# Optimization experiments

Measured on AMD Instinct MI355X. Metric: run time of the kernel, lower is better.

## Reference

```python
import jax, jax.numpy as jnp
import numpy as np

B, S, D = 4, 4096, 64

def setup_inputs() -> dict:
    key = jax.random.key(0)
    ks = jax.random.split(key, 6)
    mk = lambda k: jax.random.normal(k, (B, S, D), dtype=jnp.float32)
    return {
        "q_re": mk(ks[0]), "q_im": mk(ks[1]),
        "k_re": mk(ks[2]), "k_im": mk(ks[3]),
        "v_re": mk(ks[4]), "v_im": mk(ks[5]),
    }

def reference(q_re, q_im, k_re, k_im, v_re, v_im):
    # Complex QK^T (no conjugate, matching torch.bmm on complex tensors):
    # (qr + i qi)(kr + i ki)^T -> re = qr kr^T - qi ki^T ; im = qr ki^T + qi kr^T
    d_k = q_re.shape[-1]
    scale = 1.0 / jnp.sqrt(jnp.asarray(d_k, dtype=q_re.dtype))
    s_re = (jnp.einsum('bqd,bkd->bqk', q_re, k_re)
            - jnp.einsum('bqd,bkd->bqk', q_im, k_im)) * scale
    s_im = (jnp.einsum('bqd,bkd->bqk', q_re, k_im)
            + jnp.einsum('bqd,bkd->bqk', q_im, k_re)) * scale
    # softmax over |scores| along key axis; weights are real (imag part is 0)
    w = jax.nn.softmax(jnp.sqrt(s_re * s_re + s_im * s_im), axis=-1)  # [B,S,S]
    # CVDropout is identity in eval mode. Output = real_weights @ complex_values
    o_re = jnp.einsum('bqk,bkd->bqd', w, v_re)
    o_im = jnp.einsum('bqk,bkd->bqd', w, v_im)
    return jnp.stack([o_re, o_im], axis=0)  # [2, B, S, D] (real, imag)
```

## Files before the change

### kernel.cpp

```cpp
#include <hip/hip_runtime.h>
#include <stdint.h>

#define B_    4
#define S_    4096
#define D_    64
#define QBLK  64
#define KVBLK 64
#define NT    (S_ / KVBLK)
#define NELEM (B_ * S_ * D_)
#define BS_   (B_ * S_)

typedef __attribute__((ext_vector_type(8))) short bf16x8;
typedef __attribute__((ext_vector_type(4))) short bf16x4;
typedef __attribute__((ext_vector_type(4))) float f32x4;
typedef __attribute__((ext_vector_type(4))) int   i32x4;
typedef __attribute__((ext_vector_type(4))) unsigned u32x4;
typedef __attribute__((ext_vector_type(4))) _Float16 f16x4;

#define MFMA(a, b, c) __builtin_amdgcn_mfma_f32_16x16x32_bf16(a, b, c, 0, 0, 0)
#define VMWAIT(n) asm volatile("s_waitcnt vmcnt(" #n ")" ::: "memory")
#define BARRIER() do { asm volatile("" ::: "memory"); __builtin_amdgcn_s_barrier(); asm volatile("" ::: "memory"); } while (0)
#define LGKM_FENCE() do { asm volatile("s_waitcnt lgkmcnt(0)" ::: "memory"); __builtin_amdgcn_sched_barrier(0); } while (0)

__device__ __forceinline__ short f2bf(float x) {
    unsigned u = __builtin_bit_cast(unsigned, x);
    u += 0x7FFFu + ((u >> 16) & 1u);
    return (short)(u >> 16);
}

__device__ __forceinline__ unsigned cvtpk(float lo, float hi) {
    unsigned r;
    asm("v_cvt_pk_bf16_f32 %0, %1, %2" : "=v"(r) : "v"(lo), "v"(hi));
    return r;
}

__device__ __forceinline__ void async16(const short* g, short* l) {
    __builtin_amdgcn_global_load_lds(
        (const __attribute__((address_space(1))) unsigned int*)g,
        (__attribute__((address_space(3))) unsigned int*)l, 16, 0, 0);
}

__global__ __launch_bounds__(256)
void prepass_kernel(const float* __restrict__ q_re, const float* __restrict__ q_im,
                    const float* __restrict__ k_re, const float* __restrict__ k_im,
                    const float* __restrict__ v_re, const float* __restrict__ v_im,
                    short* __restrict__ ws) {
    const int bidx = blockIdx.x;
    const int tid  = threadIdx.x;
    if (bidx < 4096) {
        const int idx = bidx * 256 + tid;
        const int tn  = idx >> 18;
        const int e4  = idx & ((1 << 18) - 1);
        const float* s = (tn == 0 ? q_re : tn == 1 ? q_im : tn == 2 ? k_re : k_im)
                         + (size_t)e4 * 4;
        const float sc = (tn < 2) ? 0.125f : 1.0f;
        f32x4 x = *(const f32x4*)s;
        bf16x4 v;
#pragma unroll
        for (int c = 0; c < 4; ++c) v[c] = f2bf(x[c] * sc);
        *(bf16x4*)(ws + (size_t)tn * NELEM + (size_t)e4 * 4) = v;
    } else {
        __shared__ short tile[64][72];
        const int tb   = bidx - 4096;
        const int sb   = tb & 63;
        const int b    = (tb >> 6) & 3;
        const int comp = tb >> 8;
        const float* src = comp ? v_im : v_re;
        short* dst = ws + (size_t)(4 + comp) * NELEM;
#pragma unroll
        for (int i = 0; i < 4; ++i) {
            const int slot = i * 256 + tid;
            const int s  = slot >> 4;
            const int d4 = slot & 15;
            f32x4 x = *(const f32x4*)(src + (((size_t)b * S_) + sb * 64 + s) * D_ + d4 * 4);
#pragma unroll
            for (int c = 0; c < 4; ++c) tile[d4 * 4 + c][s] = f2bf(x[c]);
        }
        __syncthreads();
#pragma unroll
        for (int i = 0; i < 2; ++i) {
            const int slot = i * 256 + tid;
            const int d = slot >> 3;
            const int m = slot & 7;
            const int a = m >> 2, hh = m & 3;
            bf16x8 v;
#pragma unroll
            for (int j = 0; j < 8; ++j)
                v[j] = tile[d][a * 32 + hh * 4 + ((j >> 2) << 4) + (j & 3)];
            *(bf16x8*)(dst + ((size_t)b * 64 + d) * S_ + sb * 64 + m * 8) = v;
        }
    }
}

template<int SPLIT, typename OT>
__global__ __launch_bounds__(256, 2)
void cv_attn_main(const short* __restrict__ wsb,
                  float* __restrict__ out,
                  OT* __restrict__ opart,
                  float* __restrict__ ml)
{
    __shared__ __align__(16) short smem[2 * 4 * KVBLK * D_];

    const int tid  = threadIdx.x;
    const int lane = tid & 63;
    const int wv   = tid >> 6;
    const int l15  = lane & 15;
    const int h    = lane >> 4;

    int bid = blockIdx.x;
    const int nwg = B_ * 64 * SPLIT;
    bid = (bid & 7) * (nwg >> 3) + (bid >> 3);
    const int qb = bid & 63;
    const int sp = (bid >> 6) % SPLIT;
    const int b  = bid / (64 * SPLIT);

    const short* qr  = wsb;
    const short* qi  = wsb + (size_t)NELEM;
    const short* kr  = wsb + 2 * (size_t)NELEM;
    const short* ki  = wsb + 3 * (size_t)NELEM;
    const short* vrT = wsb + 4 * (size_t)NELEM;
    const short* viT = wsb + 5 * (size_t)NELEM;

    short* kb0 = smem + l15 * 64 + ((h ^ (l15 & 7)) << 3);
    short* kb1 = smem + l15 * 64 + (((h ^ 4) ^ (l15 & 7)) << 3);

    const int qrow = qb * QBLK + wv * 16 + l15;
    const size_t qoff = ((size_t)b * S_ + qrow) * D_;
    bf16x8 fqr[2], fqi[2], fqn[2];
#pragma unroll
    for (int dh = 0; dh < 2; ++dh) {
        fqr[dh] = *(const bf16x8*)(qr + qoff + dh * 32 + h * 8);
        fqi[dh] = *(const bf16x8*)(qi + qoff + dh * 32 + h * 8);
        i32x4 n = __builtin_bit_cast(i32x4, fqi[dh]) ^ (int)0x80008000;
        fqn[dh] = __builtin_bit_cast(bf16x8, n);
    }

    f32x4 o_re[4], o_im[4];
#pragma unroll
    for (int i = 0; i < 4; ++i) {
        o_re[i] = (f32x4){0.f, 0.f, 0.f, 0.f};
        o_im[i] = (f32x4){0.f, 0.f, 0.f, 0.f};
    }
    float m_run = -1e30f, l_run = 0.f;
    const float L2E = 1.44269504088896f;

    const int r8   = lane >> 3;
    const int u16l = lane & 7;
    constexpr int TPB = NT / SPLIT;

    auto stage = [&](int t, int DST) {
        const int kb = (sp * TPB + t) * KVBLK;
#pragma unroll
        for (int i = 0; i < 2; ++i) {
            const int row   = wv * 16 + i * 8 + r8;
            const int lbase = (wv * 16 + i * 8) * 64;
            const int swz   = (u16l ^ (row & 7)) << 3;
            const size_t koff = ((size_t)b * S_ + kb + row) * 64 + swz;
            async16(kr + koff, smem + DST + lbase);
            async16(ki + koff, smem + DST + 4096 + lbase);
            const size_t voff = ((size_t)b * 64 + row) * S_ + kb + swz;
            async16(vrT + voff, smem + DST + 8192 + lbase);
            async16(viT + voff, smem + DST + 12288 + lbase);
        }
    };

    auto body = [&](int t, int CUR, int OTH) {
        VMWAIT(0);
        LGKM_FENCE();
        BARRIER();
        if (t + 1 < TPB) stage(t + 1, OTH);

        f32x4 s_re[4], s_im[4];
#pragma unroll
        for (int c = 0; c < 4; ++c) {
            s_re[c] = (f32x4){0.f, 0.f, 0.f, 0.f};
            s_im[c] = (f32x4){0.f, 0.f, 0.f, 0.f};
        }
        __builtin_amdgcn_s_setprio(1);
#pragma unroll
        for (int c = 0; c < 4; ++c) {
            bf16x8 fkr0 = *(const bf16x8*)(kb0 + CUR + c * 1024);
            bf16x8 fkr1 = *(const bf16x8*)(kb1 + CUR + c * 1024);
            bf16x8 fki0 = *(const bf16x8*)(kb0 + CUR + 4096 + c * 1024);
            bf16x8 fki1 = *(const bf16x8*)(kb1 + CUR + 4096 + c * 1024);
            s_re[c] = MFMA(fkr0, fqr[0], s_re[c]);
            s_re[c] = MFMA(fkr1, fqr[1], s_re[c]);
            s_re[c] = MFMA(fki0, fqn[0], s_re[c]);
            s_re[c] = MFMA(fki1, fqn[1], s_re[c]);
            s_im[c] = MFMA(fki0, fqr[0], s_im[c]);
            s_im[c] = MFMA(fki1, fqr[1], s_im[c]);
            s_im[c] = MFMA(fkr0, fqi[0], s_im[c]);
            s_im[c] = MFMA(fkr1, fqi[1], s_im[c]);
        }
        __builtin_amdgcn_s_setprio(0);

#pragma unroll
        for (int c = 0; c < 4; ++c) {
            f32x4 g = s_re[c] * s_re[c] + s_im[c] * s_im[c];
#pragma unroll
            for (int r = 0; r < 4; ++r) s_re[c][r] = __builtin_amdgcn_sqrtf(g[r]);
        }
        float tmax = s_re[0][0];
#pragma unroll
        for (int c = 0; c < 4; ++c)
#pragma unroll
            for (int r = 0; r < 4; ++r) tmax = fmaxf(tmax, s_re[c][r]);
        tmax = fmaxf(tmax, __shfl_xor(tmax, 16));
        tmax = fmaxf(tmax, __shfl_xor(tmax, 32));

        if (__any(tmax > m_run + 8.0f)) {
            const float m_new = fmaxf(m_run, tmax);
            const float alpha = __builtin_amdgcn_exp2f((m_run - m_new) * L2E);
            l_run *= alpha;
#pragma unroll
            for (int i = 0; i < 4; ++i) { o_re[i] *= alpha; o_im[i] *= alpha; }
            m_run = m_new;
        }
        const float nm = -m_run * L2E;

#pragma unroll
        for (int c = 0; c < 4; ++c)
#pragma unroll
            for (int r = 0; r < 4; ++r)
                s_im[c][r] = __builtin_amdgcn_exp2f(__builtin_fmaf(s_re[c][r], L2E, nm));
        f32x4 ps = s_im[0] + s_im[1] + s_im[2] + s_im[3];
        l_run += (ps[0] + ps[1]) + (ps[2] + ps[3]);

        bf16x8 pb[2];
#pragma unroll
        for (int hf = 0; hf < 2; ++hf) {
            u32x4 w;
            w[0] = cvtpk(s_im[hf * 2][0],     s_im[hf * 2][1]);
            w[1] = cvtpk(s_im[hf * 2][2],     s_im[hf * 2][3]);
            w[2] = cvtpk(s_im[hf * 2 + 1][0], s_im[hf * 2 + 1][1]);
            w[3] = cvtpk(s_im[hf * 2 + 1][2], s_im[hf * 2 + 1][3]);
            pb[hf] = __builtin_bit_cast(bf16x8, w);
        }

        __builtin_amdgcn_s_setprio(1);
#pragma unroll
        for (int hf = 0; hf < 2; ++hf) {
            const short* kbh = hf ? kb1 : kb0;
#pragma unroll
            for (int dc = 0; dc < 4; ++dc) {
                bf16x8 av = *(const bf16x8*)(kbh + CUR + 8192  + dc * 1024);
                bf16x8 ai = *(const bf16x8*)(kbh + CUR + 12288 + dc * 1024);
                o_re[dc] = MFMA(av, pb[hf], o_re[dc]);
                o_im[dc] = MFMA(ai, pb[hf], o_im[dc]);
            }
        }
        __builtin_amdgcn_s_setprio(0);
    };

    stage(0, 0);
    for (int tt = 0; tt < TPB; tt += 2) {
        body(tt,     0,     16384);
        body(tt + 1, 16384, 0);
    }

    float lt = l_run;
    lt += __shfl_xor(lt, 16);
    lt += __shfl_xor(lt, 32);
    const float inv = 1.0f / lt;

    float* ol = (float*)smem;

    OT* dst_re;
    OT* dst_im;
    if constexpr (SPLIT == 1) {
        dst_re = (OT*)out + ((size_t)b * S_ + qb * QBLK) * D_;
        dst_im = dst_re + (size_t)NELEM;
    } else {
        const size_t qo = ((size_t)b * S_ + qb * QBLK) * D_;
        dst_re = opart + ((size_t)sp * 2 + 0) * NELEM + qo;
        dst_im = opart + ((size_t)sp * 2 + 1) * NELEM + qo;
    }

    auto store_comp = [&](const f32x4 (&oc)[4], OT* og) {
        __syncthreads();
#pragma unroll
        for (int dc = 0; dc < 4; ++dc)
#pragma unroll
            for (int r = 0; r < 4; ++r)
                ol[(wv * 16 + l15) * 65 + dc * 16 + h * 4 + r] = oc[dc][r] * inv;
        __syncthreads();
#pragma unroll
        for (int i = 0; i < 4; ++i) {
            const int slot = i * 256 + tid;
            const int row  = slot >> 4;
            const int c4   = slot & 15;
            f32x4 v;
#pragma unroll
            for (int j = 0; j < 4; ++j) v[j] = ol[row * 65 + c4 * 4 + j];
            if constexpr (sizeof(OT) == 4) {
                *(f32x4*)((float*)og + (size_t)row * D_ + c4 * 4) = v;
            } else {
                f16x4 hv;
#pragma unroll
                for (int j = 0; j < 4; ++j) hv[j] = (_Float16)v[j];
                *(f16x4*)((_Float16*)og + (size_t)row * D_ + c4 * 4) = hv;
            }
        }
    };
    store_comp(o_re, dst_re);
    store_comp(o_im, dst_im);

    if constexpr (SPLIT > 1) {
        if (lane < 16) {
            const int row = qb * QBLK + wv * 16 + lane;
            const size_t mo = ((size_t)sp * BS_ + (size_t)b * S_ + row) * 2;
            ml[mo]     = m_run;
            ml[mo + 1] = lt;
        }
    }
}

template<int SPLIT, typename OT>
__global__ __launch_bounds__(256)
void cv_attn_combine(const OT* __restrict__ opart, const float* __restrict__ ml,
                     float* __restrict__ out) {
    const int idx  = blockIdx.x * 256 + threadIdx.x;
    const int d4   = idx & 15;
    const int rest = idx >> 4;
    const int row  = rest & (BS_ - 1);
    const int comp = rest >> 14;
    float ms[SPLIT], ls[SPLIT];
    float M = -1e30f;
#pragma unroll
    for (int s = 0; s < SPLIT; ++s) {
        ms[s] = ml[((size_t)s * BS_ + row) * 2];
        ls[s] = ml[((size_t)s * BS_ + row) * 2 + 1];
        M = fmaxf(M, ms[s]);
    }
    float W = 0.f;
    f32x4 acc = (f32x4){0.f, 0.f, 0.f, 0.f};
#pragma unroll
    for (int s = 0; s < SPLIT; ++s) {
        const float w = ls[s] * __builtin_amdgcn_exp2f((ms[s] - M) * 1.44269504088896f);
        W += w;
        const OT* op = opart + ((size_t)(s * 2 + comp)) * NELEM + (size_t)row * D_ + d4 * 4;
        f32x4 o;
        if constexpr (sizeof(OT) == 4) {
            o = *(const f32x4*)op;
        } else {
            f16x4 hv = *(const f16x4*)op;
#pragma unroll
            for (int j = 0; j < 4; ++j) o[j] = (float)hv[j];
        }
        acc += o * w;
    }
    acc *= (1.0f / W);
    *(f32x4*)(out + (size_t)comp * NELEM + (size_t)row * D_ + d4 * 4) = acc;
}

__global__ __launch_bounds__(256, 1)
void cv_attn_legacy(const float* __restrict__ q_re, const float* __restrict__ q_im,
                    const float* __restrict__ k_re, const float* __restrict__ k_im,
                    const float* __restrict__ v_re, const float* __restrict__ v_im,
                    float* __restrict__ out)
{
    __shared__ __align__(16) short smem[4 * KVBLK * D_];
    short* kr_s = smem;
    short* ki_s = smem + 4096;
    short* vr_s = smem + 8192;
    short* vi_s = smem + 12288;

    const int tid  = threadIdx.x;
    const int lane = tid & 63;
    const int wv   = tid >> 6;
    const int l15  = lane & 15;
    const int h    = lane >> 4;

    const int b  = blockIdx.x >> 6;
    const int qb = blockIdx.x & 63;
    const size_t boff = (size_t)b * S_ * D_;

    const int qrow = qb * QBLK + wv * 16 + l15;
    const float* qrp = q_re + boff + (size_t)qrow * D_;
    const float* qip = q_im + boff + (size_t)qrow * D_;
    bf16x8 fqr[2], fqi[2], fqn[2];
#pragma unroll
    for (int dh = 0; dh < 2; ++dh) {
        const int d0 = dh * 32 + h * 8;
        f32x4 a0 = *(const f32x4*)(qrp + d0);
        f32x4 a1 = *(const f32x4*)(qrp + d0 + 4);
        f32x4 b0 = *(const f32x4*)(qip + d0);
        f32x4 b1 = *(const f32x4*)(qip + d0 + 4);
#pragma unroll
        for (int j = 0; j < 4; ++j) {
            fqr[dh][j] = f2bf(a0[j]); fqr[dh][j + 4] = f2bf(a1[j]);
            fqi[dh][j] = f2bf(b0[j]); fqi[dh][j + 4] = f2bf(b1[j]);
            fqn[dh][j] = f2bf(-b0[j]); fqn[dh][j + 4] = f2bf(-b1[j]);
        }
    }

    f32x4 o_re[4], o_im[4];
#pragma unroll
    for (int i = 0; i < 4; ++i) {
        o_re[i] = (f32x4){0.f, 0.f, 0.f, 0.f};
        o_im[i] = (f32x4){0.f, 0.f, 0.f, 0.f};
    }
    float m_run = -1e30f, l_run = 0.f;
    const float SC = 0.125f * 1.44269504088896f;

    for (int t = 0; t < NT; ++t) {
        const int kb = t * KVBLK;
#pragma unroll
        for (int a = 0; a < 2; ++a) {
            const float* src = (a ? k_im : k_re) + boff;
            short* dst = a ? ki_s : kr_s;
#pragma unroll
            for (int i = 0; i < 2; ++i) {
                const int slot = i * 256 + tid;
                const int row  = slot >> 3;
                const int cb   = slot & 7;
                const float* p = src + (size_t)(kb + row) * D_ + cb * 8;
                f32x4 x0 = *(const f32x4*)p;
                f32x4 x1 = *(const f32x4*)(p + 4);
                bf16x8 v;
#pragma unroll
                for (int j = 0; j < 4; ++j) { v[j] = f2bf(x0[j]); v[j + 4] = f2bf(x1[j]); }
                *(bf16x8*)(dst + row * 64 + ((cb ^ (row & 7)) << 3)) = v;
            }
        }
#pragma unroll
        for (int a = 0; a < 2; ++a) {
            const float* src = (a ? v_im : v_re) + boff;
            short* dst = a ? vi_s : vr_s;
#pragma unroll
            for (int i = 0; i < 4; ++i) {
                const int slot = i * 256 + tid;
                const int k  = slot >> 4;
                const int d4 = slot & 15;
                f32x4 x = *(const f32x4*)(src + (size_t)(kb + k) * D_ + d4 * 4);
#pragma unroll
                for (int c = 0; c < 4; ++c) {
                    const int d = d4 * 4 + c;
                    dst[d * 64 + (((k >> 2) ^ (d & 15)) << 2) + (k & 3)] = f2bf(x[c]);
                }
            }
        }
        __syncthreads();

        f32x4 s_re[4], s_im[4];
#pragma unroll
        for (int c = 0; c < 4; ++c) {
            s_re[c] = (f32x4){0.f, 0.f, 0.f, 0.f};
            s_im[c] = (f32x4){0.f, 0.f, 0.f, 0.f};
        }
#pragma unroll
        for (int c = 0; c < 4; ++c) {
            const int krow = c * 16 + l15;
#pragma unroll
            for (int dh = 0; dh < 2; ++dh) {
                const int u = ((dh * 4 + h) ^ (krow & 7)) << 3;
                bf16x8 fkr = *(const bf16x8*)(kr_s + krow * 64 + u);
                bf16x8 fki = *(const bf16x8*)(ki_s + krow * 64 + u);
                s_re[c] = MFMA(fkr, fqr[dh], s_re[c]);
                s_re[c] = MFMA(fki, fqn[dh], s_re[c]);
                s_im[c] = MFMA(fki, fqr[dh], s_im[c]);
                s_im[c] = MFMA(fkr, fqi[dh], s_im[c]);
            }
        }

        float pv[4][4];
        float tmax = 0.f;
#pragma unroll
        for (int c = 0; c < 4; ++c)
#pragma unroll
            for (int r = 0; r < 4; ++r) {
                const float re = s_re[c][r], im = s_im[c][r];
                const float mg = __builtin_amdgcn_sqrtf(re * re + im * im) * SC;
                pv[c][r] = mg;
                tmax = fmaxf(tmax, mg);
            }
        tmax = fmaxf(tmax, __shfl_xor(tmax, 16));
        tmax = fmaxf(tmax, __shfl_xor(tmax, 32));
        const float m_new = fmaxf(m_run, tmax);
        const float alpha = __builtin_amdgcn_exp2f(m_run - m_new);
        m_run = m_new;
        float psum = 0.f;
#pragma unroll
        for (int c = 0; c < 4; ++c)
#pragma unroll
            for (int r = 0; r < 4; ++r) {
                const float e = __builtin_amdgcn_exp2f(pv[c][r] - m_new);
                pv[c][r] = e;
                psum += e;
            }
        l_run = l_run * alpha + psum;
#pragma unroll
        for (int i = 0; i < 4; ++i) { o_re[i] *= alpha; o_im[i] *= alpha; }

        bf16x8 pb[2];
#pragma unroll
        for (int hf = 0; hf < 2; ++hf)
#pragma unroll
            for (int j = 0; j < 4; ++j) {
                pb[hf][j]     = f2bf(pv[hf * 2][j]);
                pb[hf][j + 4] = f2bf(pv[hf * 2 + 1][j]);
            }

#pragma unroll
        for (int hf = 0; hf < 2; ++hf) {
#pragma unroll
            for (int dc = 0; dc < 4; ++dc) {
                const int d  = dc * 16 + l15;
                const int s0 = (((hf * 8) + h)     ^ l15) << 2;
                const int s1 = (((hf * 8) + 4 + h) ^ l15) << 2;
                bf16x4 r0 = *(const bf16x4*)(vr_s + d * 64 + s0);
                bf16x4 r1 = *(const bf16x4*)(vr_s + d * 64 + s1);
                bf16x4 i0 = *(const bf16x4*)(vi_s + d * 64 + s0);
                bf16x4 i1 = *(const bf16x4*)(vi_s + d * 64 + s1);
                bf16x8 av, ai;
#pragma unroll
                for (int j = 0; j < 4; ++j) {
                    av[j] = r0[j]; av[j + 4] = r1[j];
                    ai[j] = i0[j]; ai[j + 4] = i1[j];
                }
                o_re[dc] = MFMA(av, pb[hf], o_re[dc]);
                o_im[dc] = MFMA(ai, pb[hf], o_im[dc]);
            }
        }
        __syncthreads();
    }

    float lt = l_run;
    lt += __shfl_xor(lt, 16);
    lt += __shfl_xor(lt, 32);
    const float inv = 1.0f / lt;

    float* ol = (float*)smem;
    auto store_comp = [&](const f32x4 (&oc)[4], float* og) {
#pragma unroll
        for (int dc = 0; dc < 4; ++dc)
#pragma unroll
            for (int r = 0; r < 4; ++r)
                ol[(wv * 16 + l15) * 65 + dc * 16 + h * 4 + r] = oc[dc][r] * inv;
        __syncthreads();
#pragma unroll
        for (int i = 0; i < 4; ++i) {
            const int slot = i * 256 + tid;
            const int row  = slot >> 4;
            const int c4   = slot & 15;
            f32x4 v;
#pragma unroll
            for (int j = 0; j < 4; ++j) v[j] = ol[row * 65 + c4 * 4 + j];
            *(f32x4*)(og + (size_t)row * D_ + c4 * 4) = v;
        }
        __syncthreads();
    };

    float* og0 = out + boff + (size_t)(qb * QBLK) * D_;
    store_comp(o_re, og0);
    store_comp(o_im, og0 + (size_t)B_ * S_ * D_);
}

extern "C" void kernel_launch(void* const* d_in, const int* in_sizes, int n_in,
                              void* d_out, int out_size, void* d_ws, size_t ws_size,
                              hipStream_t stream) {
    (void)in_sizes; (void)n_in; (void)out_size;
    const float* q_re = (const float*)d_in[0];
    const float* q_im = (const float*)d_in[1];
    const float* k_re = (const float*)d_in[2];
    const float* k_im = (const float*)d_in[3];
    const float* v_re = (const float*)d_in[4];
    const float* v_im = (const float*)d_in[5];
    float* out = (float*)d_out;

    const size_t bf_bytes = 6 * (size_t)NELEM * 2;
    const size_t mlsz     = 4 * (size_t)BS_ * 8;
    const size_t need4f16 = bf_bytes + 4 * 2 * (size_t)NELEM * 2 + mlsz;
    const size_t need4f32 = bf_bytes + 4 * 2 * (size_t)NELEM * 4 + mlsz;

    if (ws_size >= bf_bytes) {
        short* wsb = (short*)d_ws;
        prepass_kernel<<<4608, 256, 0, stream>>>(q_re, q_im, k_re, k_im, v_re, v_im, wsb);
        char* extra = (char*)d_ws + bf_bytes;
        if (ws_size >= need4f16) {
            _Float16* opart = (_Float16*)extra;
            float* ml = (float*)(extra + 4 * 2 * (size_t)NELEM * 2);
            cv_attn_main<4, _Float16><<<B_ * 64 * 4, 256, 0, stream>>>(wsb, nullptr, opart, ml);
            cv_attn_combine<4, _Float16><<<2048, 256, 0, stream>>>(opart, ml, out);
        } else if (ws_size >= need4f32) {
            float* opart = (float*)extra;
            float* ml    = (float*)(extra + 4 * 2 * (size_t)NELEM * 4);
            cv_attn_main<4, float><<<B_ * 64 * 4, 256, 0, stream>>>(wsb, nullptr, opart, ml);
            cv_attn_combine<4, float><<<2048, 256, 0, stream>>>(opart, ml, out);
        } else {
            cv_attn_main<1, float><<<B_ * 64, 256, 0, stream>>>(wsb, out, out, nullptr);
        }
    } else {
        cv_attn_legacy<<<B_ * 64, 256, 0, stream>>>(q_re, q_im, k_re, k_im, v_re, v_im, out);
    }
}
```

Baseline: 81.02 us.

## Halve KV tile to 32 rows to shrink LDS and raise occupancy

```diff
diff --git a/kernel.cpp b/kernel.cpp
--- a/kernel.cpp
+++ b/kernel.cpp
@@ -5,8 +5,6 @@
 #define S_    4096
 #define D_    64
 #define QBLK  64
-#define KVBLK 64
-#define NT    (S_ / KVBLK)
 #define NELEM (B_ * S_ * D_)
 #define BS_   (B_ * S_)
 
@@ -93,13 +91,13 @@
 }
 
 template<int SPLIT, typename OT>
-__global__ __launch_bounds__(256, 2)
+__global__ __launch_bounds__(256, 4)
 void cv_attn_main(const short* __restrict__ wsb,
                   float* __restrict__ out,
                   OT* __restrict__ opart,
                   float* __restrict__ ml)
 {
-    __shared__ __align__(16) short smem[2 * 4 * KVBLK * D_];
+    __shared__ __align__(16) short smem[2 * 8192];
 
     const int tid  = threadIdx.x;
     const int lane = tid & 63;
@@ -123,6 +121,7 @@
 
     short* kb0 = smem + l15 * 64 + ((h ^ (l15 & 7)) << 3);
     short* kb1 = smem + l15 * 64 + (((h ^ 4) ^ (l15 & 7)) << 3);
+    short* vb0 = smem + l15 * 32 + ((h ^ (l15 & 3)) << 3);
 
     const int qrow = qb * QBLK + wv * 16 + l15;
     const size_t qoff = ((size_t)b * S_ + qrow) * D_;
@@ -144,24 +143,20 @@
     float m_run = -1e30f, l_run = 0.f;
     const float L2E = 1.44269504088896f;
 
-    const int r8   = lane >> 3;
-    const int u16l = lane & 7;
-    constexpr int TPB = NT / SPLIT;
+    const int kRow = wv * 8 + (lane >> 3);
+    const int u8   = lane & 7;
+    const int vD   = wv * 16 + (lane >> 2);
+    const int u4   = lane & 3;
+    constexpr int TPB = (S_ / 32) / SPLIT;
 
     auto stage = [&](int t, int DST) {
-        const int kb = (sp * TPB + t) * KVBLK;
-#pragma unroll
-        for (int i = 0; i < 2; ++i) {
-            const int row   = wv * 16 + i * 8 + r8;
-            const int lbase = (wv * 16 + i * 8) * 64;
-            const int swz   = (u16l ^ (row & 7)) << 3;
-            const size_t koff = ((size_t)b * S_ + kb + row) * 64 + swz;
-            async16(kr + koff, smem + DST + lbase);
-            async16(ki + koff, smem + DST + 4096 + lbase);
-            const size_t voff = ((size_t)b * 64 + row) * S_ + kb + swz;
-            async16(vrT + voff, smem + DST + 8192 + lbase);
-            async16(viT + voff, smem + DST + 12288 + lbase);
-        }
+        const int kb = (sp * TPB + t) * 32;
+        const size_t koff = ((size_t)b * S_ + kb + kRow) * 64 + ((u8 ^ (kRow & 7)) << 3);
+        async16(kr + koff, smem + DST + wv * 512);
+        async16(ki + koff, smem + DST + 2048 + wv * 512);
+        const size_t voff = ((size_t)b * 64 + vD) * S_ + kb + ((u4 ^ (vD & 3)) << 3);
+        async16(vrT + voff, smem + DST + 4096 + wv * 512);
+        async16(viT + voff, smem + DST + 6144 + wv * 512);
     };
 
     auto body = [&](int t, int CUR, int OTH) {
@@ -170,19 +165,19 @@
         BARRIER();
         if (t + 1 < TPB) stage(t + 1, OTH);
 
-        f32x4 s_re[4], s_im[4];
-#pragma unroll
-        for (int c = 0; c < 4; ++c) {
+        f32x4 s_re[2], s_im[2];
+#pragma unroll
+        for (int c = 0; c < 2; ++c) {
             s_re[c] = (f32x4){0.f, 0.f, 0.f, 0.f};
             s_im[c] = (f32x4){0.f, 0.f, 0.f, 0.f};
         }
         __builtin_amdgcn_s_setprio(1);
 #pragma unroll
-        for (int c = 0; c < 4; ++c) {
+        for (int c = 0; c < 2; ++c) {
             bf16x8 fkr0 = *(const bf16x8*)(kb0 + CUR + c * 1024);
             bf16x8 fkr1 = *(const bf16x8*)(kb1 + CUR + c * 1024);
-            bf16x8 fki0 = *(const bf16x8*)(kb0 + CUR + 4096 + c * 1024);
-            bf16x8 fki1 = *(const bf16x8*)(kb1 + CUR + 4096 + c * 1024);
+            bf16x8 fki0 = *(const bf16x8*)(kb0 + CUR + 2048 + c * 1024);
+            bf16x8 fki1 = *(const bf16x8*)(kb1 + CUR + 2048 + c * 1024);
             s_re[c] = MFMA(fkr0, fqr[0], s_re[c]);
             s_re[c] = MFMA(fkr1, fqr[1], s_re[c]);
             s_re[c] = MFMA(fki0, fqn[0], s_re[c]);
@@ -195,16 +190,13 @@
         __builtin_amdgcn_s_setprio(0);
 
 #pragma unroll
-        for (int c = 0; c < 4; ++c) {
+        for (int c = 0; c < 2; ++c) {
             f32x4 g = s_re[c] * s_re[c] + s_im[c] * s_im[c];
 #pragma unroll
             for (int r = 0; r < 4; ++r) s_re[c][r] = __builtin_amdgcn_sqrtf(g[r]);
         }
-        float tmax = s_re[0][0];
-#pragma unroll
-        for (int c = 0; c < 4; ++c)
-#pragma unroll
-            for (int r = 0; r < 4; ++r) tmax = fmaxf(tmax, s_re[c][r]);
+        float tmax = fmaxf(fmaxf(fmaxf(s_re[0][0], s_re[0][1]), fmaxf(s_re[0][2], s_re[0][3])),
+                           fmaxf(fmaxf(s_re[1][0], s_re[1][1]), fmaxf(s_re[1][2], s_re[1][3])));
         tmax = fmaxf(tmax, __shfl_xor(tmax, 16));
         tmax = fmaxf(tmax, __shfl_xor(tmax, 32));
 
@@ -219,43 +211,35 @@
         const float nm = -m_run * L2E;
 
 #pragma unroll
-        for (int c = 0; c < 4; ++c)
+        for (int c = 0; c < 2; ++c)
 #pragma unroll
             for (int r = 0; r < 4; ++r)
                 s_im[c][r] = __builtin_amdgcn_exp2f(__builtin_fmaf(s_re[c][r], L2E, nm));
-        f32x4 ps = s_im[0] + s_im[1] + s_im[2] + s_im[3];
+        f32x4 ps = s_im[0] + s_im[1];
         l_run += (ps[0] + ps[1]) + (ps[2] + ps[3]);
 
-        bf16x8 pb[2];
-#pragma unroll
-        for (int hf = 0; hf < 2; ++hf) {
-            u32x4 w;
-            w[0] = cvtpk(s_im[hf * 2][0],     s_im[hf * 2][1]);
-            w[1] = cvtpk(s_im[hf * 2][2],     s_im[hf * 2][3]);
-            w[2] = cvtpk(s_im[hf * 2 + 1][0], s_im[hf * 2 + 1][1]);
-            w[3] = cvtpk(s_im[hf * 2 + 1][2], s_im[hf * 2 + 1][3]);
-            pb[hf] = __builtin_bit_cast(bf16x8, w);
-        }
+        u32x4 w;
+        w[0] = cvtpk(s_im[0][0], s_im[0][1]);
+        w[1] = cvtpk(s_im[0][2], s_im[0][3]);
+        w[2] = cvtpk(s_im[1][0], s_im[1][1]);
+        w[3] = cvtpk(s_im[1][2], s_im[1][3]);
+        bf16x8 pb = __builtin_bit_cast(bf16x8, w);
 
         __builtin_amdgcn_s_setprio(1);
 #pragma unroll
-        for (int hf = 0; hf < 2; ++hf) {
-            const short* kbh = hf ? kb1 : kb0;
-#pragma unroll
-            for (int dc = 0; dc < 4; ++dc) {
-                bf16x8 av = *(const bf16x8*)(kbh + CUR + 8192  + dc * 1024);
-                bf16x8 ai = *(const bf16x8*)(kbh + CUR + 12288 + dc * 1024);
-                o_re[dc] = MFMA(av, pb[hf], o_re[dc]);
-                o_im[dc] = MFMA(ai, pb[hf], o_im[dc]);
-            }
+        for (int dc = 0; dc < 4; ++dc) {
+            bf16x8 av = *(const bf16x8*)(vb0 + CUR + 4096 + dc * 512);
+            bf16x8 ai = *(const bf16x8*)(vb0 + CUR + 6144 + dc * 512);
+            o_re[dc] = MFMA(av, pb, o_re[dc]);
+            o_im[dc] = MFMA(ai, pb, o_im[dc]);
         }
         __builtin_amdgcn_s_setprio(0);
     };
 
     stage(0, 0);
     for (int tt = 0; tt < TPB; tt += 2) {
-        body(tt,     0,     16384);
-        body(tt + 1, 16384, 0);
+        body(tt,     0,    8192);
+        body(tt + 1, 8192, 0);
     }
 
     float lt = l_run;
@@ -359,7 +343,7 @@
                     const float* __restrict__ v_re, const float* __restrict__ v_im,
                     float* __restrict__ out)
 {
-    __shared__ __align__(16) short smem[4 * KVBLK * D_];
+    __shared__ __align__(16) short smem[4 * 64 * D_];
     short* kr_s = smem;
     short* ki_s = smem + 4096;
     short* vr_s = smem + 8192;
@@ -403,8 +387,8 @@
     float m_run = -1e30f, l_run = 0.f;
     const float SC = 0.125f * 1.44269504088896f;
 
-    for (int t = 0; t < NT; ++t) {
-        const int kb = t * KVBLK;
+    for (int t = 0; t < S_ / 64; ++t) {
+        const int kb = t * 64;
 #pragma unroll
         for (int a = 0; a < 2; ++a) {
             const float* src = (a ? k_im : k_re) + boff;
```

Result: no change. 80.41 us (-0.8%).
